# Performance work log

Measured on AMD Instinct MI355X. Metric: run time of the kernel, lower is better.

Reference implementation:

```python
import jax, jax.numpy as jnp
import numpy as np

T = 10
EPS = 1e-05

def setup_inputs() -> dict:
    key = jax.random.key(0)
    k1, k2 = jax.random.split(key)
    B, C, H, W = 128, 64, 56, 56
    X = jax.random.normal(k1, (B, C, H, W), dtype=jnp.float32)
    beta = jnp.zeros((C,), dtype=jnp.float32)
    return {"X": X, "beta": beta}


def reference(X, beta):
    # Training-path of BWItnBlock.forward (grad enabled branch of iter_norm_batch)
    B, C, H, W = X.shape
    d = C                      # n_channels, num_groups g = 1
    m = B * H * W
    # x = X.transpose(0,1).view(g, d, -1)  -> [d, m] with g=1
    x = jnp.transpose(X, (1, 0, 2, 3)).reshape(d, m)
    mean = jnp.mean(x, axis=1, keepdims=True)          # [d, 1]
    xc = x - mean                                      # [d, m]
    I = jnp.eye(d, dtype=X.dtype)
    # Sigma = eps*I + xc xc^T / m
    Sigma = EPS * I + (xc @ xc.T) / m                  # [d, d]
    # fix_cov: multiply off-diagonal by 0.9, diagonal by 1.0
    fix = 0.9 + 0.1 * I
    Sigma = Sigma * fix
    rTr = 1.0 / jnp.trace(Sigma)                       # scalar (sum(Sigma * I))
    Sigma_N = Sigma * rTr
    # Newton-Schulz iterations for inverse sqrt: P <- 1.5 P - 0.5 P^3 Sigma_N
    P = I
    for _ in range(T):
        P = 1.5 * P - 0.5 * ((P @ P @ P) @ Sigma_N)
    wm = P * jnp.sqrt(rTr)                             # whitening matrix [d, d]
    xn = wm @ xc                                       # [d, m]
    X_hat = jnp.transpose(xn.reshape(C, B, H, W), (1, 0, 2, 3))
    X_hat = X_hat + beta.reshape(1, C, 1, 1)
    return X_hat
```

## Files before the change

kernel.cpp:

```cpp
#include <hip/hip_runtime.h>

#define CH 64
#define HW 3136
#define MTOT 401408
#define TPX 128
#define K1_NBLK 784
#define K1_TPB 4

typedef __attribute__((ext_vector_type(8))) short short8;
typedef __attribute__((ext_vector_type(4))) float f32x4;
typedef __attribute__((ext_vector_type(4))) unsigned int u32x4;

__device__ __forceinline__ void split8(const float4 a, const float4 b,
                                       short8& hi, short8& lo, float& ssum){
  const float f[8] = {a.x,a.y,a.z,a.w, b.x,b.y,b.z,b.w};
  u32x4 hp, lp;
#pragma unroll
  for (int j=0;j<4;++j){
    const unsigned int b0 = __float_as_uint(f[2*j]);
    const unsigned int b1 = __float_as_uint(f[2*j+1]);
    hp[j] = (b0 >> 16) | (b1 & 0xFFFF0000u);
    const float h0 = __uint_as_float(b0 & 0xFFFF0000u);
    const float h1 = __uint_as_float(b1 & 0xFFFF0000u);
    const unsigned int l0 = __float_as_uint(f[2*j]   - h0);
    const unsigned int l1 = __float_as_uint(f[2*j+1] - h1);
    lp[j] = (l0 >> 16) | (l1 & 0xFFFF0000u);
  }
  hi = __builtin_bit_cast(short8, hp);
  lo = __builtin_bit_cast(short8, lp);
  ssum += ((f[0]+f[1])+(f[2]+f[3])) + ((f[4]+f[5])+(f[6]+f[7]));
}

__global__ __launch_bounds__(256) void k1_cov(const float* __restrict__ X,
                                              float* __restrict__ SR){
  constexpr int RG[10] = {0,1,1,2,2,2,3,3,3,3};
  constexpr int CG[10] = {0,0,1,0,1,2,0,1,2,3};
  __shared__ __align__(16) float buf[2][64*TPX];
  __shared__ float chs[64];

  const int t   = threadIdx.x;
  const int wid = __builtin_amdgcn_readfirstlane(t >> 6);
  const int l   = t & 63;
  const int lr  = l & 15;
  const int q   = l >> 4;

  f32x4 acc[10];
#pragma unroll
  for (int bi=0; bi<10; ++bi) acc[bi] = (f32x4){0.f,0.f,0.f,0.f};
  float sums[4] = {0.f,0.f,0.f,0.f};

  auto stage = [&](int tl, float* dst){
    const unsigned mbase = (unsigned)(blockIdx.x*K1_TPB + tl) * TPX;
#pragma unroll
    for (int j=0;j<8;++j){
      const int r  = 16*wid + 2*j + (l>>5);
      const int cb = (l&31) ^ (r&7);
      const unsigned m  = mbase + 4*cb;
      const unsigned b  = m / HW;
      const unsigned hw = m - b*HW;
      const float* src = X + (size_t)b*(CH*HW) + (size_t)r*HW + hw;
      __builtin_amdgcn_global_load_lds(
        (const __attribute__((address_space(1))) unsigned int*)src,
        (__attribute__((address_space(3))) unsigned int*)(dst + (16*wid + 2*j)*TPX),
        16, 0, 0);
    }
  };

  stage(0, buf[0]);
  asm volatile("s_waitcnt vmcnt(0)" ::: "memory");
  __syncthreads();

  int pb = 0;
  for (int tl=0; tl<K1_TPB; ++tl){
    if (tl+1 < K1_TPB) stage(tl+1, buf[pb^1]);
    const char* bp = (const char*)buf[pb];
    short8 fh[4], fl[4];
#pragma unroll
    for (int g=0; g<4; ++g){
      const int r   = 16*g + lr;
      const int sw  = r & 7;
      const int cb0 = 8*wid + 2*q;
      const float4 v0 = *(const float4*)(bp + r*512 + 16*((cb0+0)^sw));
      const float4 v1 = *(const float4*)(bp + r*512 + 16*((cb0+1)^sw));
      split8(v0, v1, fh[g], fl[g], sums[g]);
    }
#pragma unroll
    for (int bi=0; bi<10; ++bi){
      acc[bi] = __builtin_amdgcn_mfma_f32_16x16x32_bf16(fh[RG[bi]], fh[CG[bi]], acc[bi], 0,0,0);
      acc[bi] = __builtin_amdgcn_mfma_f32_16x16x32_bf16(fh[RG[bi]], fl[CG[bi]], acc[bi], 0,0,0);
      acc[bi] = __builtin_amdgcn_mfma_f32_16x16x32_bf16(fl[RG[bi]], fh[CG[bi]], acc[bi], 0,0,0);
    }
    asm volatile("s_waitcnt vmcnt(0)" ::: "memory");
    __syncthreads();
    pb ^= 1;
  }

#pragma unroll
  for (int g=0; g<4; ++g){
    sums[g] += __shfl_xor(sums[g], 16);
    sums[g] += __shfl_xor(sums[g], 32);
  }

  float* red = &buf[0][0];
  for (int w=0; w<4; ++w){
    if (wid == w){
#pragma unroll
      for (int bi=0; bi<10; ++bi){
        const int row0 = RG[bi]*16 + 4*q;
        const int col  = CG[bi]*16 + lr;
#pragma unroll
        for (int r=0; r<4; ++r){
          float* d = &red[(row0+r)*64 + col];
          if (w==0) *d = acc[bi][r]; else *d += acc[bi][r];
        }
      }
      if (l < 16){
#pragma unroll
        for (int g=0; g<4; ++g){
          if (w==0) chs[g*16+l] = sums[g]; else chs[g*16+l] += sums[g];
        }
      }
    }
    __syncthreads();
  }

#pragma unroll
  for (int bi=0; bi<10; ++bi){
    const int r = RG[bi]*16 + (t>>4);
    const int c = CG[bi]*16 + (t&15);
    unsafeAtomicAdd(&SR[r*64+c], red[r*64+c]);
  }
  if (t < 64) unsafeAtomicAdd(&SR[4096+t], chs[t]);
}

__device__ __forceinline__ void mm_AtB(const float* a, const float* b, float* out,
                                       float alpha, const float* aff, float beta_){
  const int t = threadIdx.x;
  const int c2 = 2*(t & 31);
  const int r0 = 8*(t >> 5);
  float acc[8][2];
#pragma unroll
  for (int i=0;i<8;++i){ acc[i][0]=0.f; acc[i][1]=0.f; }
  for (int k=0;k<64;++k){
    const float2 bv = *(const float2*)&b[k*64 + c2];
    const float4 a0 = *(const float4*)&a[k*64 + r0];
    const float4 a1 = *(const float4*)&a[k*64 + r0 + 4];
    const float av[8] = {a0.x,a0.y,a0.z,a0.w, a1.x,a1.y,a1.z,a1.w};
#pragma unroll
    for (int i=0;i<8;++i){ acc[i][0] += av[i]*bv.x; acc[i][1] += av[i]*bv.y; }
  }
  float res[8][2];
#pragma unroll
  for (int i=0;i<8;++i){
    float f0 = alpha*acc[i][0], f1 = alpha*acc[i][1];
    if (aff){ f0 += beta_*aff[(r0+i)*64 + c2]; f1 += beta_*aff[(r0+i)*64 + c2 + 1]; }
    res[i][0]=f0; res[i][1]=f1;
  }
  __syncthreads();
#pragma unroll
  for (int i=0;i<8;++i){
    float2 o2; o2.x = res[i][0]; o2.y = res[i][1];
    *(float2*)&out[(r0+i)*64 + c2] = o2;
  }
  __syncthreads();
}

__global__ __launch_bounds__(256) void k2_wm(const float* __restrict__ SR,
                                             const float* __restrict__ beta,
                                             float* __restrict__ WM,
                                             float* __restrict__ OFS){
  __shared__ __align__(16) float bufE[4096];
  __shared__ __align__(16) float bufA[4096];
  __shared__ __align__(16) float bufB[4096];
  __shared__ float meanv[64];
  __shared__ float scal[2];
  const int t = threadIdx.x;
  const float inv_m = 1.f/(float)MTOT;
  if (t < 64) meanv[t] = SR[4096 + t]*inv_m;
  __syncthreads();
  for (int idx=t; idx<4096; idx+=256){
    const int r = idx >> 6, c = idx & 63;
    const int src = ((r >> 4) >= (c >> 4)) ? idx : (c*64 + r);
    const float cov = SR[src]*inv_m - meanv[r]*meanv[c];
    bufE[idx] = (r==c) ? (cov + 1e-5f - 1.f) : 0.9f*cov;
  }
  __syncthreads();
  float n2 = 0.f, tr = 0.f;
  for (int idx=t; idx<4096; idx+=256){
    const float e = bufE[idx];
    n2 += e*e;
    if ((idx >> 6) == (idx & 63)) tr += e;
  }
  bufA[t] = n2; bufB[t] = tr;
  __syncthreads();
  if (t < 64){
    bufA[t] = bufA[t]+bufA[t+64]+bufA[t+128]+bufA[t+192];
    bufB[t] = bufB[t]+bufB[t+64]+bufB[t+128]+bufB[t+192];
  }
  __syncthreads();
  if (t == 0){
    float s1=0.f, s2=0.f;
    for (int i=0;i<64;++i){ s1 += bufA[i]; s2 += bufB[i]; }
    scal[0] = s1; scal[1] = s2;
  }
  __syncthreads();
  const float frob2 = scal[0];
  const float trE   = scal[1];
  float wscale = 1.f;
  const float* wmLds;
  if (frob2 < 0.04f){
    mm_AtB(bufE, bufE, bufA, 1.f, nullptr, 0.f);
    mm_AtB(bufA, bufE, bufB, 1.f, nullptr, 0.f);
    for (int idx=t; idx<4096; idx+=256){
      const int r = idx >> 6, c = idx & 63;
      bufB[idx] = ((r==c)?1.f:0.f) - 0.5f*bufE[idx] + 0.375f*bufA[idx] - 0.3125f*bufB[idx];
    }
    mm_AtB(bufA, bufA, bufE, 1.f, nullptr, 0.f);
    for (int idx=t; idx<4096; idx+=256)
      bufB[idx] += 0.2734375f*bufE[idx];
    wmLds = bufB;
  } else {
    const float rTr = 1.f/(trE + 64.f);
    for (int idx=t; idx<4096; idx+=256){
      const int r = idx >> 6, c = idx & 63;
      bufE[idx] = (bufE[idx] + ((r==c)?1.f:0.f))*rTr;
      bufA[idx] = (r==c)?1.f:0.f;
    }
    __syncthreads();
    for (int it=0; it<10; ++it){
      mm_AtB(bufA, bufE, bufB, 1.f, nullptr, 0.f);
      mm_AtB(bufA, bufB, bufB, 1.f, nullptr, 0.f);
      mm_AtB(bufA, bufB, bufA, -0.5f, bufA, 1.5f);
    }
    wscale = sqrtf(rTr);
    wmLds = bufA;
  }
  __syncthreads();
  for (int idx=t; idx<4096; idx+=256) WM[idx] = wmLds[idx]*wscale;
  if (t < 64){
    float d = 0.f;
    for (int j=0;j<64;++j) d += wmLds[t*64 + j]*meanv[j];
    OFS[t] = beta[t] - d*wscale;
  }
}

__global__ __launch_bounds__(256) void k3_apply(const float* __restrict__ X,
                                                const float* __restrict__ WM,
                                                const float* __restrict__ OFS,
                                                float* __restrict__ out){
  const int t   = threadIdx.x;
  const int wid = __builtin_amdgcn_readfirstlane(t >> 6);
  const int l   = t & 63;
  const int lr  = l & 15;
  const int q   = l >> 4;

  short8 ah[4][2], al[4][2];
  float dummy = 0.f;
#pragma unroll
  for (int cb=0; cb<4; ++cb)
#pragma unroll
    for (int ks=0; ks<2; ++ks){
      const float* wp = WM + (16*cb + lr)*64 + ks*32 + q*8;
      const float4 w0 = *(const float4*)wp;
      const float4 w1 = *(const float4*)(wp + 4);
      split8(w0, w1, ah[cb][ks], al[cb][ks], dummy);
    }

  unsigned bb[2], hwp[2];
#pragma unroll
  for (int pbk=0; pbk<2; ++pbk){
    const unsigned px = (unsigned)blockIdx.x*128u + 32u*wid + 16u*pbk + lr;
    bb[pbk]  = px / HW;
    hwp[pbk] = px - bb[pbk]*HW;
  }

  f32x4 acc[4][2];
#pragma unroll
  for (int cb=0; cb<4; ++cb)
#pragma unroll
    for (int pbk=0; pbk<2; ++pbk) acc[cb][pbk] = (f32x4){0.f,0.f,0.f,0.f};

#pragma unroll
  for (int ks=0; ks<2; ++ks){
    short8 bh[2], bl[2];
#pragma unroll
    for (int pbk=0; pbk<2; ++pbk){
      const float* xb = X + (size_t)bb[pbk]*(CH*HW) + hwp[pbk] + (size_t)(ks*32 + q*8)*HW;
      float f[8];
#pragma unroll
      for (int j=0;j<8;++j) f[j] = xb[(size_t)j*HW];
      const float4 v0 = {f[0],f[1],f[2],f[3]};
      const float4 v1 = {f[4],f[5],f[6],f[7]};
      split8(v0, v1, bh[pbk], bl[pbk], dummy);
    }
#pragma unroll
    for (int cb=0; cb<4; ++cb)
#pragma unroll
      for (int pbk=0; pbk<2; ++pbk){
        acc[cb][pbk] = __builtin_amdgcn_mfma_f32_16x16x32_bf16(ah[cb][ks], bh[pbk], acc[cb][pbk], 0,0,0);
        acc[cb][pbk] = __builtin_amdgcn_mfma_f32_16x16x32_bf16(ah[cb][ks], bl[pbk], acc[cb][pbk], 0,0,0);
        acc[cb][pbk] = __builtin_amdgcn_mfma_f32_16x16x32_bf16(al[cb][ks], bh[pbk], acc[cb][pbk], 0,0,0);
      }
  }

#pragma unroll
  for (int cb=0; cb<4; ++cb){
    float ofs[4];
#pragma unroll
    for (int r=0;r<4;++r) ofs[r] = OFS[16*cb + 4*q + r];
#pragma unroll
    for (int pbk=0; pbk<2; ++pbk){
      float* ob = out + (size_t)bb[pbk]*(CH*HW) + hwp[pbk] + (size_t)(16*cb + 4*q)*HW;
#pragma unroll
      for (int r=0;r<4;++r)
        ob[(size_t)r*HW] = acc[cb][pbk][r] + ofs[r];
    }
  }
}

extern "C" void kernel_launch(void* const* d_in, const int* in_sizes, int n_in,
                              void* d_out, int out_size, void* d_ws, size_t ws_size,
                              hipStream_t stream){
  const float* X    = (const float*)d_in[0];
  const float* beta = (const float*)d_in[1];
  float* out = (float*)d_out;
  float* ws  = (float*)d_ws;
  float* SR  = ws;
  float* WM  = ws + 4160;
  float* OFS = WM + 4096;
  hipMemsetAsync(SR, 0, 4160*sizeof(float), stream);
  hipLaunchKernelGGL(k1_cov,   dim3(K1_NBLK), dim3(256), 0, stream, X, SR);
  hipLaunchKernelGGL(k2_wm,    dim3(1),       dim3(256), 0, stream, SR, beta, WM, OFS);
  hipLaunchKernelGGL(k3_apply, dim3(3136),    dim3(256), 0, stream, X, WM, OFS, out);
}
```

Measured before the change: 230.4 us.

## Stage apply-kernel inputs through LDS with double-buffered async loads

The apply kernel now loads X tiles into double-buffered shared memory with global_load_lds and processes four 128-pixel tiles per block (784 blocks instead of 3136). Per-channel strided global reads become coalesced async loads, overlapped with MFMA work through partial vmcnt waits. The covariance kernel's pipeline drops the full vmcnt(0)+syncthreads in favour of partial waits and raw s_barrier. This relies on hand-set vmcnt counts that must account for the interleaved output stores, and it adds 64KB of LDS per block, which limits occupancy.

```diff
diff --git a/kernel.cpp b/kernel.cpp
--- a/kernel.cpp
+++ b/kernel.cpp
@@ -4,8 +4,8 @@
 #define HW 3136
 #define MTOT 401408
 #define TPX 128
-#define K1_NBLK 784
-#define K1_TPB 4
+#define NBLK 784
+#define TPB 4
 
 typedef __attribute__((ext_vector_type(8))) short short8;
 typedef __attribute__((ext_vector_type(4))) float f32x4;
@@ -50,7 +50,7 @@
   float sums[4] = {0.f,0.f,0.f,0.f};
 
   auto stage = [&](int tl, float* dst){
-    const unsigned mbase = (unsigned)(blockIdx.x*K1_TPB + tl) * TPX;
+    const unsigned mbase = (unsigned)(blockIdx.x*TPB + tl) * TPX;
 #pragma unroll
     for (int j=0;j<8;++j){
       const int r  = 16*wid + 2*j + (l>>5);
@@ -67,12 +67,17 @@
   };
 
   stage(0, buf[0]);
-  asm volatile("s_waitcnt vmcnt(0)" ::: "memory");
-  __syncthreads();
-
   int pb = 0;
-  for (int tl=0; tl<K1_TPB; ++tl){
-    if (tl+1 < K1_TPB) stage(tl+1, buf[pb^1]);
+#pragma unroll
+  for (int tl=0; tl<TPB; ++tl){
+    if (tl+1 < TPB){
+      stage(tl+1, buf[pb^1]);
+      asm volatile("s_waitcnt vmcnt(8)" ::: "memory");
+    } else {
+      asm volatile("s_waitcnt vmcnt(0)" ::: "memory");
+    }
+    __builtin_amdgcn_sched_barrier(0);
+    asm volatile("s_barrier" ::: "memory");
     const char* bp = (const char*)buf[pb];
     short8 fh[4], fl[4];
 #pragma unroll
@@ -90,8 +95,7 @@
       acc[bi] = __builtin_amdgcn_mfma_f32_16x16x32_bf16(fh[RG[bi]], fl[CG[bi]], acc[bi], 0,0,0);
       acc[bi] = __builtin_amdgcn_mfma_f32_16x16x32_bf16(fl[RG[bi]], fh[CG[bi]], acc[bi], 0,0,0);
     }
-    asm volatile("s_waitcnt vmcnt(0)" ::: "memory");
-    __syncthreads();
+    asm volatile("s_barrier" ::: "memory");
     pb ^= 1;
   }
 
@@ -248,6 +252,7 @@
                                                 const float* __restrict__ WM,
                                                 const float* __restrict__ OFS,
                                                 float* __restrict__ out){
+  __shared__ __align__(16) float buf[2][64*TPX];
   const int t   = threadIdx.x;
   const int wid = __builtin_amdgcn_readfirstlane(t >> 6);
   const int l   = t & 63;
@@ -265,56 +270,90 @@
       const float4 w1 = *(const float4*)(wp + 4);
       split8(w0, w1, ah[cb][ks], al[cb][ks], dummy);
     }
-
-  unsigned bb[2], hwp[2];
-#pragma unroll
-  for (int pbk=0; pbk<2; ++pbk){
-    const unsigned px = (unsigned)blockIdx.x*128u + 32u*wid + 16u*pbk + lr;
-    bb[pbk]  = px / HW;
-    hwp[pbk] = px - bb[pbk]*HW;
-  }
-
-  f32x4 acc[4][2];
+  float ofsv[4][4];
 #pragma unroll
   for (int cb=0; cb<4; ++cb)
 #pragma unroll
-    for (int pbk=0; pbk<2; ++pbk) acc[cb][pbk] = (f32x4){0.f,0.f,0.f,0.f};
-
-#pragma unroll
-  for (int ks=0; ks<2; ++ks){
-    short8 bh[2], bl[2];
-#pragma unroll
-    for (int pbk=0; pbk<2; ++pbk){
-      const float* xb = X + (size_t)bb[pbk]*(CH*HW) + hwp[pbk] + (size_t)(ks*32 + q*8)*HW;
-      float f[8];
-#pragma unroll
-      for (int j=0;j<8;++j) f[j] = xb[(size_t)j*HW];
-      const float4 v0 = {f[0],f[1],f[2],f[3]};
-      const float4 v1 = {f[4],f[5],f[6],f[7]};
-      split8(v0, v1, bh[pbk], bl[pbk], dummy);
-    }
+    for (int r=0; r<4; ++r) ofsv[cb][r] = OFS[16*cb + 4*q + r];
+
+  auto stage = [&](int tl, float* dst){
+    const unsigned mbase = (unsigned)(blockIdx.x*TPB + tl) * TPX;
+#pragma unroll
+    for (int j=0;j<8;++j){
+      const int r = 16*wid + 2*j + (l>>5);
+      const unsigned pxs = 4*(l&31);
+      const unsigned m  = mbase + (pxs ^ (((r>>3)&1u)<<4));
+      const unsigned b  = m / HW;
+      const unsigned hw = m - b*HW;
+      const float* src = X + (size_t)b*(CH*HW) + (size_t)r*HW + hw;
+      __builtin_amdgcn_global_load_lds(
+        (const __attribute__((address_space(1))) unsigned int*)src,
+        (__attribute__((address_space(3))) unsigned int*)(dst + (16*wid + 2*j)*TPX),
+        16, 0, 0);
+    }
+  };
+
+  stage(0, buf[0]);
+  int pb = 0;
+#pragma unroll
+  for (int tl=0; tl<TPB; ++tl){
+    if (tl+1 < TPB) stage(tl+1, buf[pb^1]);
+    if (tl == 0)          asm volatile("s_waitcnt vmcnt(8)"  ::: "memory");
+    else if (tl+1 < TPB)  asm volatile("s_waitcnt vmcnt(40)" ::: "memory");
+    else                  asm volatile("s_waitcnt vmcnt(32)" ::: "memory");
+    __builtin_amdgcn_sched_barrier(0);
+    asm volatile("s_barrier" ::: "memory");
+
+    const float* bp = buf[pb];
+    f32x4 acc[4][2];
 #pragma unroll
     for (int cb=0; cb<4; ++cb)
 #pragma unroll
-      for (int pbk=0; pbk<2; ++pbk){
-        acc[cb][pbk] = __builtin_amdgcn_mfma_f32_16x16x32_bf16(ah[cb][ks], bh[pbk], acc[cb][pbk], 0,0,0);
-        acc[cb][pbk] = __builtin_amdgcn_mfma_f32_16x16x32_bf16(ah[cb][ks], bl[pbk], acc[cb][pbk], 0,0,0);
-        acc[cb][pbk] = __builtin_amdgcn_mfma_f32_16x16x32_bf16(al[cb][ks], bh[pbk], acc[cb][pbk], 0,0,0);
+      for (int pk=0; pk<2; ++pk) acc[cb][pk] = (f32x4){0.f,0.f,0.f,0.f};
+
+#pragma unroll
+    for (int ks=0; ks<2; ++ks){
+      short8 bh[2], bl[2];
+#pragma unroll
+      for (int pk=0; pk<2; ++pk){
+        const int ch0 = ks*32 + q*8;
+        const int pxl = 32*wid + 16*pk + lr;
+        const int pxs = pxl ^ ((q&1)<<4);
+        const float* rp = bp + ch0*TPX + pxs;
+        float f[8];
+#pragma unroll
+        for (int j=0;j<8;++j) f[j] = rp[j*TPX];
+        const float4 v0 = {f[0],f[1],f[2],f[3]};
+        const float4 v1 = {f[4],f[5],f[6],f[7]};
+        split8(v0, v1, bh[pk], bl[pk], dummy);
       }
-  }
-
-#pragma unroll
-  for (int cb=0; cb<4; ++cb){
-    float ofs[4];
-#pragma unroll
-    for (int r=0;r<4;++r) ofs[r] = OFS[16*cb + 4*q + r];
-#pragma unroll
-    for (int pbk=0; pbk<2; ++pbk){
-      float* ob = out + (size_t)bb[pbk]*(CH*HW) + hwp[pbk] + (size_t)(16*cb + 4*q)*HW;
-#pragma unroll
-      for (int r=0;r<4;++r)
-        ob[(size_t)r*HW] = acc[cb][pbk][r] + ofs[r];
-    }
+#pragma unroll
+      for (int cb=0; cb<4; ++cb)
+#pragma unroll
+        for (int pk=0; pk<2; ++pk){
+          acc[cb][pk] = __builtin_amdgcn_mfma_f32_16x16x32_bf16(ah[cb][ks], bh[pk], acc[cb][pk], 0,0,0);
+          acc[cb][pk] = __builtin_amdgcn_mfma_f32_16x16x32_bf16(ah[cb][ks], bl[pk], acc[cb][pk], 0,0,0);
+          acc[cb][pk] = __builtin_amdgcn_mfma_f32_16x16x32_bf16(al[cb][ks], bh[pk], acc[cb][pk], 0,0,0);
+        }
+    }
+
+    {
+      const unsigned mbase = (unsigned)(blockIdx.x*TPB + tl) * TPX;
+#pragma unroll
+      for (int pk=0; pk<2; ++pk){
+        const unsigned P  = mbase + 32*wid + 16*pk + lr;
+        const unsigned b2 = P / HW;
+        const unsigned hw2 = P - b2*HW;
+        float* ob = out + (size_t)b2*(CH*HW) + hw2 + (size_t)(4*q)*HW;
+#pragma unroll
+        for (int cb=0; cb<4; ++cb)
+#pragma unroll
+          for (int r=0; r<4; ++r)
+            ob[(size_t)(16*cb + r)*HW] = acc[cb][pk][r] + ofsv[cb][r];
+      }
+    }
+    asm volatile("s_barrier" ::: "memory");
+    pb ^= 1;
   }
 }
 
@@ -329,7 +368,7 @@
   float* WM  = ws + 4160;
   float* OFS = WM + 4096;
   hipMemsetAsync(SR, 0, 4160*sizeof(float), stream);
-  hipLaunchKernelGGL(k1_cov,   dim3(K1_NBLK), dim3(256), 0, stream, X, SR);
-  hipLaunchKernelGGL(k2_wm,    dim3(1),       dim3(256), 0, stream, SR, beta, WM, OFS);
-  hipLaunchKernelGGL(k3_apply, dim3(3136),    dim3(256), 0, stream, X, WM, OFS, out);
-}
+  hipLaunchKernelGGL(k1_cov,   dim3(NBLK), dim3(256), 0, stream, X, SR);
+  hipLaunchKernelGGL(k2_wm,    dim3(1),    dim3(256), 0, stream, SR, beta, WM, OFS);
+  hipLaunchKernelGGL(k3_apply, dim3(NBLK), dim3(256), 0, stream, X, WM, OFS, out);
+}
```

New measurement: 239.4 us. 1.04x slower.
